# Kernel tuning notes

Measured on AMD Instinct MI355X. Metric: run time of the kernel, lower is better.

## Reference

```python
import jax, jax.numpy as jnp
import numpy as np
from jax import lax

B, T, D, LD, K = 128, 1024, 256, 512, 128
RD = LD + K  # 640 residual-LSTM width
PAD = 15     # (31 - 1) // 2 'same' padding for the LSA location conv


def _gru(x, h, wih, whh, bih, bhh):
    # torch.nn.GRUCell semantics, gate order [r, z, n]
    gi = x @ wih.T + bih
    gh = h @ whh.T + bhh
    ir, iz, inn = jnp.split(gi, 3, axis=-1)
    hr, hz, hn = jnp.split(gh, 3, axis=-1)
    r = jax.nn.sigmoid(ir + hr)
    z = jax.nn.sigmoid(iz + hz)
    n = jnp.tanh(inn + r * hn)
    return (1.0 - z) * n + z * h


def _lstm(x, h, c, wih, whh, bih, bhh):
    # torch.nn.LSTMCell semantics, gate order [i, f, g, o]
    g = x @ wih.T + bih + h @ whh.T + bhh
    i, f, gg, o = jnp.split(g, 4, axis=-1)
    c2 = jax.nn.sigmoid(f) * c + jax.nn.sigmoid(i) * jnp.tanh(gg)
    h2 = jax.nn.sigmoid(o) * jnp.tanh(c2)
    return h2, c2


def _forward(encoder_seq, encoder_seq_proj, prenet_in, attn_hidden, rnn1_h, rnn1_c,
             rnn2_h, rnn2_c, res_h, res_c, context_vec, cumulative, attn_prev,
             fc1_w, fc1_b, fc2_w, fc2_b, gru_wih, gru_whh, gru_bih, gru_bhh,
             conv_w, L_w, L_b, W_w, W_b, v_w, ri_w, ri_b,
             r1_wih, r1_whh, r1_bih, r1_bhh, r2_wih, r2_whh, r2_bih, r2_bhh,
             res_wih, res_whh, res_bih, res_bhh, stop_w, stop_b):
    # PreNet (dropout p = 0 in Decoder.__init__, so pure tanh-MLP)
    p = jnp.tanh(prenet_in @ fc1_w.T + fc1_b)
    prenet_out = jnp.tanh(p @ fc2_w.T + fc2_b)                     # [B, D//2]
    # Attention GRU
    attn_in = jnp.concatenate([context_vec, prenet_out], axis=-1)  # [B, D + D//2]
    attn_h = _gru(attn_in, attn_hidden, gru_wih, gru_whh, gru_bih, gru_bhh)  # [B, D]
    # LSA location-sensitive attention (cumulative/attn_prev are zeros at t=0)
    pq = (attn_h @ W_w.T + W_b)[:, None, :]                        # [B, 1, D]
    loc = jnp.stack([cumulative, attn_prev], axis=1)               # [B, 2, T]
    conv_out = lax.conv_general_dilated(loc, conv_w, (1,), [(PAD, PAD)],
                                        dimension_numbers=('NCH', 'OIH', 'NCH'))  # [B, 32, T]
    ploc = jnp.swapaxes(conv_out, 1, 2) @ L_w.T + L_b              # [B, T, D]
    u = jnp.squeeze(jnp.tanh(pq + encoder_seq_proj + ploc) @ v_w.T, -1)  # [B, T]
    sig = jax.nn.sigmoid(u)
    scores = sig / jnp.sum(sig, axis=1, keepdims=True)             # [B, T]
    cum_new = cumulative + scores
    context = jnp.einsum('bt,btd->bd', scores, encoder_seq)        # [B, D]
    # rnn_input projection + two residual LSTM cells (eval: no zoneout)
    x = jnp.concatenate([context, attn_h], axis=1) @ ri_w.T + ri_b  # [B, LD]
    h1, c1 = _lstm(x, rnn1_h, rnn1_c, r1_wih, r1_whh, r1_bih, r1_bhh)
    x = x + h1
    h2, c2 = _lstm(x, rnn2_h, rnn2_c, r2_wih, r2_whh, r2_bih, r2_bhh)
    x = x + h2
    # 4-layer residual LSTM stack on [prenet_in, x]
    res_x = jnp.concatenate([prenet_in, x], axis=1)                # [B, RD]
    hs, cs = [], []
    for i in range(4):
        hi, ci = _lstm(res_x, res_h[i], res_c[i], res_wih[i], res_whh[i], res_bih[i], res_bhh[i])
        res_x = res_x + hi
        hs.append(hi)
        cs.append(ci)
    cond = res_x                                                   # cond_features [B, RD]
    stop = jax.nn.sigmoid(cond @ stop_w.T + stop_b)                # [B, 1]
    return (cond, stop, scores, attn_h, h1, c1, h2, c2,
            jnp.stack(hs), jnp.stack(cs), context, cum_new)


def setup_inputs() -> dict:
    keys = iter(jax.random.split(jax.random.key(0), 64))
    nxt = lambda: next(keys)
    rn = lambda s: jax.random.normal(nxt(), s, jnp.float32)
    wp = lambda s: rn(s) * 0.02
    return {
        'encoder_seq': rn((B, T, D)),
        'encoder_seq_proj': rn((B, T, D)),
        'prenet_in': rn((B, K)),
        'attn_hidden': rn((B, D)),
        'rnn1_h': rn((B, LD)), 'rnn1_c': rn((B, LD)),
        'rnn2_h': rn((B, LD)), 'rnn2_c': rn((B, LD)),
        'res_h': rn((4, B, RD)), 'res_c': rn((4, B, RD)),
        'context_vec': rn((B, D)),
        'cumulative': jnp.zeros((B, T), jnp.float32),
        'attn_prev': jnp.zeros((B, T), jnp.float32),
        'fc1_w': wp((256, K)), 'fc1_b': jnp.zeros((256,), jnp.float32),
        'fc2_w': wp((D // 2, 256)), 'fc2_b': jnp.zeros((D // 2,), jnp.float32),
        'gru_wih': wp((3 * D, D + D // 2)), 'gru_whh': wp((3 * D, D)),
        'gru_bih': jnp.zeros((3 * D,), jnp.float32), 'gru_bhh': jnp.zeros((3 * D,), jnp.float32),
        'conv_w': wp((32, 2, 31)),
        'L_w': wp((D, 32)), 'L_b': jnp.zeros((D,), jnp.float32),
        'W_w': wp((D, D)), 'W_b': jnp.zeros((D,), jnp.float32),
        'v_w': wp((1, D)),
        'ri_w': wp((LD, 2 * D)), 'ri_b': jnp.zeros((LD,), jnp.float32),
        'r1_wih': wp((4 * LD, LD)), 'r1_whh': wp((4 * LD, LD)),
        'r1_bih': jnp.zeros((4 * LD,), jnp.float32), 'r1_bhh': jnp.zeros((4 * LD,), jnp.float32),
        'r2_wih': wp((4 * LD, LD)), 'r2_whh': wp((4 * LD, LD)),
        'r2_bih': jnp.zeros((4 * LD,), jnp.float32), 'r2_bhh': jnp.zeros((4 * LD,), jnp.float32),
        'res_wih': wp((4, 4 * RD, RD)), 'res_whh': wp((4, 4 * RD, RD)),
        'res_bih': jnp.zeros((4, 4 * RD), jnp.float32), 'res_bhh': jnp.zeros((4, 4 * RD), jnp.float32),
        'stop_w': wp((1, RD)), 'stop_b': jnp.zeros((1,), jnp.float32),
    }


def reference(encoder_seq, encoder_seq_proj, prenet_in, attn_hidden, rnn1_h, rnn1_c,
              rnn2_h, rnn2_c, res_h, res_c, context_vec, cumulative, attn_prev,
              fc1_w, fc1_b, fc2_w, fc2_b, gru_wih, gru_whh, gru_bih, gru_bhh,
              conv_w, L_w, L_b, W_w, W_b, v_w, ri_w, ri_b,
              r1_wih, r1_whh, r1_bih, r1_bhh, r2_wih, r2_whh, r2_bih, r2_bhh,
              res_wih, res_whh, res_bih, res_bhh, stop_w, stop_b):
    return _forward(encoder_seq, encoder_seq_proj, prenet_in, attn_hidden, rnn1_h, rnn1_c,
                    rnn2_h, rnn2_c, res_h, res_c, context_vec, cumulative, attn_prev,
                    fc1_w, fc1_b, fc2_w, fc2_b, gru_wih, gru_whh, gru_bih, gru_bhh,
                    conv_w, L_w, L_b, W_w, W_b, v_w, ri_w, ri_b,
                    r1_wih, r1_whh, r1_bih, r1_bhh, r2_wih, r2_whh, r2_bih, r2_bhh,
                    res_wih, res_whh, res_bih, res_bhh, stop_w, stop_b)
```

## Files before the change

### kernel.cpp

```cpp
#include <hip/hip_runtime.h>

#define DEV __device__ __forceinline__

typedef __attribute__((ext_vector_type(8))) short short8;
typedef __attribute__((ext_vector_type(4))) float f32x4;

DEV float fast_rcp(float x) { return __builtin_amdgcn_rcpf(x); }
DEV float sigm(float x) { return fast_rcp(1.0f + __expf(-x)); }
DEV float tanhf_fast(float x) { return 1.0f - 2.0f * fast_rcp(1.0f + __expf(2.0f * x)); }

DEV short f2bf(float f) {
    unsigned u = __float_as_uint(f);
    unsigned r = (u + 0x7FFFu + ((u >> 16) & 1u)) >> 16;
    return (short)r;
}

__global__ __launch_bounds__(256) void gemm2s_kernel(
    const float* __restrict__ A1, int K1, const float* __restrict__ W1, int ldw1,
    const float* __restrict__ A2, int K2, const float* __restrict__ W2, int ldw2,
    float* __restrict__ Cp, int N, int KS, int KC)
{
    __shared__ float As[2][16][128];
    __shared__ float Ws[2][16][33];
    const int tid = threadIdx.x;
    const int chunk = blockIdx.x % KS;
    const int n0 = (blockIdx.x / KS) * 32;
    const int kbeg = chunk * KC;
    const int nt = KC / 16;
    const int tx = tid & 15, ty = tid >> 4;
    const int lm = tid & 127, lk = (tid >> 7) * 8;

    float acc[16];
#pragma unroll
    for (int i = 0; i < 16; ++i) acc[i] = 0.f;

    float4 ra0, ra1, rw;
    auto load_regs = [&](int k0) {
        const float* A; const float* W; int lda, ldw, kc;
        if (k0 < K1) { A = A1; W = W1; lda = K1; ldw = ldw1; kc = k0; }
        else         { A = A2; W = W2; lda = K2; ldw = ldw2; kc = k0 - K1; }
        ra0 = *(const float4*)(A + (size_t)lm * lda + kc + lk);
        ra1 = *(const float4*)(A + (size_t)lm * lda + kc + lk + 4);
        if (tid < 128) {
            int nl = tid >> 2, kq = (tid & 3) * 4;
            rw = *(const float4*)(W + (size_t)(n0 + nl) * ldw + kc + kq);
        }
    };
    auto store_lds = [&](int buf) {
        As[buf][lk + 0][lm] = ra0.x; As[buf][lk + 1][lm] = ra0.y;
        As[buf][lk + 2][lm] = ra0.z; As[buf][lk + 3][lm] = ra0.w;
        As[buf][lk + 4][lm] = ra1.x; As[buf][lk + 5][lm] = ra1.y;
        As[buf][lk + 6][lm] = ra1.z; As[buf][lk + 7][lm] = ra1.w;
        if (tid < 128) {
            int nl = tid >> 2, kq = (tid & 3) * 4;
            Ws[buf][kq + 0][nl] = rw.x; Ws[buf][kq + 1][nl] = rw.y;
            Ws[buf][kq + 2][nl] = rw.z; Ws[buf][kq + 3][nl] = rw.w;
        }
    };

    load_regs(kbeg);
    store_lds(0);
    __syncthreads();

    for (int it = 0; it < nt; ++it) {
        const int cur = it & 1;
        if (it + 1 < nt) load_regs(kbeg + (it + 1) * 16);
#pragma unroll
        for (int kk = 0; kk < 16; ++kk) {
            float w0 = Ws[cur][kk][tx * 2 + 0];
            float w1 = Ws[cur][kk][tx * 2 + 1];
            float4 x0 = *(const float4*)&As[cur][kk][ty * 8];
            float4 x1 = *(const float4*)&As[cur][kk][ty * 8 + 4];
            acc[0] += x0.x * w0; acc[1] += x0.y * w0;
            acc[2] += x0.z * w0; acc[3] += x0.w * w0;
            acc[4] += x1.x * w0; acc[5] += x1.y * w0;
            acc[6] += x1.z * w0; acc[7] += x1.w * w0;
            acc[8]  += x0.x * w1; acc[9]  += x0.y * w1;
            acc[10] += x0.z * w1; acc[11] += x0.w * w1;
            acc[12] += x1.x * w1; acc[13] += x1.y * w1;
            acc[14] += x1.z * w1; acc[15] += x1.w * w1;
        }
        if (it + 1 < nt) store_lds(cur ^ 1);
        __syncthreads();
    }

    float* Co = Cp + (size_t)chunk * 128 * N;
#pragma unroll
    for (int j = 0; j < 2; ++j) {
        int n = n0 + tx * 2 + j;
#pragma unroll
        for (int i = 0; i < 8; ++i)
            Co[(size_t)(ty * 8 + i) * N + n] = acc[j * 8 + i];
    }
}

__global__ void reduce_act_kernel(const float* __restrict__ p, int KS, int MN,
                                  const float* __restrict__ b,
                                  float* __restrict__ out, int N, int act)
{
    int idx = blockIdx.x * 256 + threadIdx.x;
    if (idx >= MN) return;
    int n = idx % N;
    float v = b ? b[n] : 0.f;
    for (int s = 0; s < KS; ++s) v += p[(size_t)s * MN + idx];
    if (act) v = tanhf_fast(v);
    out[idx] = v;
}

__global__ void gru_gate_kernel(const float* __restrict__ gi_p, int KSi,
                                const float* __restrict__ gh_p, int KSh,
                                const float* __restrict__ bih, const float* __restrict__ bhh,
                                const float* __restrict__ h, float* __restrict__ out)
{
    const size_t MN = 128 * 768;
    int m = blockIdx.x, d = threadIdx.x;
    size_t base = (size_t)m * 768 + d;
    float ir = bih[d], iz = bih[256 + d], in = bih[512 + d];
    for (int s = 0; s < KSi; ++s) {
        const float* p = gi_p + s * MN + base;
        ir += p[0]; iz += p[256]; in += p[512];
    }
    float hr = bhh[d], hz = bhh[256 + d], hn = bhh[512 + d];
    for (int s = 0; s < KSh; ++s) {
        const float* p = gh_p + s * MN + base;
        hr += p[0]; hz += p[256]; hn += p[512];
    }
    float r = sigm(ir + hr);
    float z = sigm(iz + hz);
    float n = tanhf_fast(in + r * hn);
    out[m * 256 + d] = (1.f - z) * n + z * h[m * 256 + d];
}

__global__ void lstm_gate_kernel(const float* __restrict__ gp, int KS,
                                 const float* __restrict__ bih, const float* __restrict__ bhh,
                                 const float* __restrict__ c_in,
                                 float* __restrict__ h_out, float* __restrict__ c_out,
                                 float* __restrict__ xacc, int H)
{
    int d = blockIdx.x * 256 + threadIdx.x;
    int m = blockIdx.y;
    if (d >= H) return;
    const size_t MN = (size_t)128 * 4 * H;
    size_t base = (size_t)m * 4 * H + d;
    float iv = bih[d] + bhh[d];
    float fv = bih[H + d] + bhh[H + d];
    float gv = bih[2 * H + d] + bhh[2 * H + d];
    float ov = bih[3 * H + d] + bhh[3 * H + d];
    for (int s = 0; s < KS; ++s) {
        const float* p = gp + s * MN + base;
        iv += p[0]; fv += p[H]; gv += p[2 * H]; ov += p[3 * H];
    }
    float c2 = sigm(fv) * c_in[m * H + d] + sigm(iv) * tanhf_fast(gv);
    float h2 = sigm(ov) * tanhf_fast(c2);
    h_out[m * H + d] = h2;
    c_out[m * H + d] = c2;
    if (xacc) xacc[m * H + d] += h2;
}

__global__ void lw_bf16_kernel(const float* __restrict__ Lw, short* __restrict__ LwBf)
{
    int i = blockIdx.x * 256 + threadIdx.x;
    LwBf[i] = f2bf(Lw[i]);
}

__global__ __launch_bounds__(256) void attn_u_kernel(
    const float* __restrict__ esp, const float* __restrict__ pq,
    const short* __restrict__ LwBf, const float* __restrict__ Lb,
    const float* __restrict__ vw, const float* __restrict__ cw,
    const float* __restrict__ cum, const float* __restrict__ prev,
    float* __restrict__ sig_out)
{
    const int b = blockIdx.x >> 4;
    const int t0 = (blockIdx.x & 15) << 6;
    const int tid = threadIdx.x;

    __shared__ float cum_s[94], prev_s[94];
    __shared__ float cw_s[2][32][33];
    __shared__ short conv_bf[64 * 32];
    __shared__ short lw_bf[256 * 32];
    __shared__ float pq_s[256], vw_s[256];

    if (tid < 94) {
        int ti = t0 - 15 + tid;
        cum_s[tid] = (ti >= 0 && ti < 1024) ? cum[b * 1024 + ti] : 0.f;
    } else if (tid >= 128 && tid < 222) {
        int i = tid - 128;
        int ti = t0 - 15 + i;
        prev_s[i] = (ti >= 0 && ti < 1024) ? prev[b * 1024 + ti] : 0.f;
    }
    for (int i = tid; i < 2048; i += 256) {
        int which = i >> 10, c = (i >> 5) & 31, k = i & 31;
        cw_s[which][c][k] = (k < 31) ? cw[(c * 2 + which) * 31 + k] : 0.f;
    }
    {
        const int4* src = (const int4*)LwBf;
        int4* dst = (int4*)lw_bf;
#pragma unroll
        for (int k = 0; k < 4; ++k) dst[tid + k * 256] = src[tid + k * 256];
    }
    pq_s[tid] = pq[b * 256 + tid] + Lb[tid];
    vw_s[tid] = vw[tid];
    __syncthreads();

    {
        int c = tid & 31, t8 = (tid >> 5) << 3;
        float a[8] = {0.f, 0.f, 0.f, 0.f, 0.f, 0.f, 0.f, 0.f};
        for (int k = 0; k < 31; ++k) {
            float w0 = cw_s[0][c][k], w1 = cw_s[1][c][k];
#pragma unroll
            for (int j = 0; j < 8; ++j)
                a[j] += w0 * cum_s[t8 + j + k] + w1 * prev_s[t8 + j + k];
        }
#pragma unroll
        for (int j = 0; j < 8; ++j) conv_bf[(t8 + j) * 32 + c] = f2bf(a[j]);
    }
    __syncthreads();

    const int lane = tid & 63, w = tid >> 6;
    const int q = lane >> 4, c16 = lane & 15;
    const int myt = t0 + w * 16 + c16;

    short8 bfrag = *(const short8*)&conv_bf[(w * 16 + c16) * 32 + q * 8];
    const float* er = esp + ((size_t)(b * 1024 + myt) << 8);

    float s = 0.f;
#pragma unroll
    for (int dt = 0; dt < 16; ++dt) {
        short8 afrag = *(const short8*)&lw_bf[(dt * 16 + c16) * 32 + q * 8];
        f32x4 acc = {0.f, 0.f, 0.f, 0.f};
        acc = __builtin_amdgcn_mfma_f32_16x16x32_bf16(afrag, bfrag, acc, 0, 0, 0);
        const int d0 = dt * 16 + q * 4;
        float4 e   = *(const float4*)(er + d0);
        float4 pqv = *(const float4*)&pq_s[d0];
        float4 vwv = *(const float4*)&vw_s[d0];
        s += tanhf_fast(pqv.x + e.x + acc[0]) * vwv.x;
        s += tanhf_fast(pqv.y + e.y + acc[1]) * vwv.y;
        s += tanhf_fast(pqv.z + e.z + acc[2]) * vwv.z;
        s += tanhf_fast(pqv.w + e.w + acc[3]) * vwv.w;
    }
    s += __shfl_xor(s, 16);
    s += __shfl_xor(s, 32);
    if (lane < 16)
        sig_out[b * 1024 + t0 + w * 16 + lane] = sigm(s);
}

__global__ void attn_norm_kernel(const float* __restrict__ sig, const float* __restrict__ cum,
                                 float* __restrict__ scores, float* __restrict__ cum_new,
                                 float* __restrict__ ctx)
{
    __shared__ float red[4];
    int b = blockIdx.x, tid = threadIdx.x;
    float4 sv = *(const float4*)&sig[b * 1024 + tid * 4];
    float s = sv.x + sv.y + sv.z + sv.w;
#pragma unroll
    for (int off = 1; off < 64; off <<= 1) s += __shfl_xor(s, off);
    if ((tid & 63) == 0) red[tid >> 6] = s;
    __syncthreads();
    float inv = fast_rcp(red[0] + red[1] + red[2] + red[3]);
    float4 cv = *(const float4*)&cum[b * 1024 + tid * 4];
    float4 sc = {sv.x * inv, sv.y * inv, sv.z * inv, sv.w * inv};
    *(float4*)&scores[b * 1024 + tid * 4] = sc;
    float4 cn = {cv.x + sc.x, cv.y + sc.y, cv.z + sc.z, cv.w + sc.w};
    *(float4*)&cum_new[b * 1024 + tid * 4] = cn;
    ctx[b * 256 + tid] = 0.f;
}

__global__ void attn_ctx_kernel(const float* __restrict__ scores, const float* __restrict__ es,
                                float* __restrict__ ctx)
{
    __shared__ float sc_s[128];
    int b = blockIdx.x >> 3;
    int tbase = (blockIdx.x & 7) * 128;
    int tid = threadIdx.x;
    if (tid < 128) sc_s[tid] = scores[b * 1024 + tbase + tid];
    __syncthreads();
    float a = 0.f;
    const float* ep = es + ((size_t)(b * 1024 + tbase)) * 256 + tid;
#pragma unroll 4
    for (int tt = 0; tt < 128; ++tt)
        a += sc_s[tt] * ep[(size_t)tt * 256];
    atomicAdd(&ctx[b * 256 + tid], a);
}

__global__ void build_rescat_kernel(const float* __restrict__ pre, const float* __restrict__ x,
                                    float* __restrict__ res)
{
    int idx = blockIdx.x * 256 + threadIdx.x;
    int m = idx / 640, d = idx - m * 640;
    res[idx] = (d < 128) ? pre[m * 128 + d] : x[m * 512 + d - 128];
}

__global__ void copy_kernel(const float* __restrict__ src, float* __restrict__ dst, int n)
{
    int idx = blockIdx.x * 256 + threadIdx.x;
    if (idx < n) dst[idx] = src[idx];
}

__global__ void stop_kernel(const float* __restrict__ res, const float* __restrict__ sw,
                            const float* __restrict__ sb, float* __restrict__ stop)
{
    int m = blockIdx.x, lane = threadIdx.x;
    float s = 0.f;
    for (int k = lane; k < 640; k += 64) s += res[m * 640 + k] * sw[k];
#pragma unroll
    for (int off = 1; off < 64; off <<= 1) s += __shfl_xor(s, off);
    if (lane == 0) stop[m] = sigm(s + sb[0]);
}

extern "C" void kernel_launch(void* const* d_in, const int* in_sizes, int n_in,
                              void* d_out, int out_size, void* d_ws, size_t ws_size,
                              hipStream_t stream)
{
    const float* encoder_seq      = (const float*)d_in[0];
    const float* encoder_seq_proj = (const float*)d_in[1];
    const float* prenet_in        = (const float*)d_in[2];
    const float* attn_hidden      = (const float*)d_in[3];
    const float* rnn1_h  = (const float*)d_in[4];
    const float* rnn1_c  = (const float*)d_in[5];
    const float* rnn2_h  = (const float*)d_in[6];
    const float* rnn2_c  = (const float*)d_in[7];
    const float* res_h   = (const float*)d_in[8];
    const float* res_c   = (const float*)d_in[9];
    const float* context_vec = (const float*)d_in[10];
    const float* cumulative  = (const float*)d_in[11];
    const float* attn_prev   = (const float*)d_in[12];
    const float* fc1_w = (const float*)d_in[13];
    const float* fc1_b = (const float*)d_in[14];
    const float* fc2_w = (const float*)d_in[15];
    const float* fc2_b = (const float*)d_in[16];
    const float* gru_wih = (const float*)d_in[17];
    const float* gru_whh = (const float*)d_in[18];
    const float* gru_bih = (const float*)d_in[19];
    const float* gru_bhh = (const float*)d_in[20];
    const float* conv_w = (const float*)d_in[21];
    const float* L_w = (const float*)d_in[22];
    const float* L_b = (const float*)d_in[23];
    const float* W_w = (const float*)d_in[24];
    const float* W_b = (const float*)d_in[25];
    const float* v_w = (const float*)d_in[26];
    const float* ri_w = (const float*)d_in[27];
    const float* ri_b = (const float*)d_in[28];
    const float* r1_wih = (const float*)d_in[29];
    const float* r1_whh = (const float*)d_in[30];
    const float* r1_bih = (const float*)d_in[31];
    const float* r1_bhh = (const float*)d_in[32];
    const float* r2_wih = (const float*)d_in[33];
    const float* r2_whh = (const float*)d_in[34];
    const float* r2_bih = (const float*)d_in[35];
    const float* r2_bhh = (const float*)d_in[36];
    const float* res_wih = (const float*)d_in[37];
    const float* res_whh = (const float*)d_in[38];
    const float* res_bih = (const float*)d_in[39];
    const float* res_bhh = (const float*)d_in[40];
    const float* stop_w = (const float*)d_in[41];
    const float* stop_b = (const float*)d_in[42];

    float* ws  = (float*)d_ws;
    float* out = (float*)d_out;

    const size_t OFF_P    = 0;
    const size_t OFF_POUT = 32768;
    const size_t OFF_PQ   = 49152;
    const size_t OFF_SIG  = 81920;
    const size_t OFF_X    = 212992;
    const size_t OFF_RES  = 278528;
    const size_t OFF_LWT  = 360448;
    const size_t OFF_PART = 368640;
    const size_t OFF_PARTB = OFF_PART + (size_t)8 * 128 * 768;

    const size_t O_COND   = 0;
    const size_t O_STOP   = 81920;
    const size_t O_SCORES = 82048;
    const size_t O_ATTNH  = 213120;
    const size_t O_H1     = 245888;
    const size_t O_C1     = 311424;
    const size_t O_H2     = 376960;
    const size_t O_C2     = 442496;
    const size_t O_HS     = 508032;
    const size_t O_CS     = 835712;
    const size_t O_CTX    = 1163392;
    const size_t O_CUM    = 1196160;

    short* lwbf = (short*)(ws + OFF_LWT);
    lw_bf16_kernel<<<32, 256, 0, stream>>>(L_w, lwbf);

    gemm2s_kernel<<<8 * 4, 256, 0, stream>>>(prenet_in, 128, fc1_w, 128,
                                             nullptr, 0, nullptr, 0,
                                             ws + OFF_PART, 256, 4, 32);
    reduce_act_kernel<<<128, 256, 0, stream>>>(ws + OFF_PART, 4, 128 * 256, fc1_b,
                                               ws + OFF_P, 256, 1);
    gemm2s_kernel<<<4 * 8, 256, 0, stream>>>(ws + OFF_P, 256, fc2_w, 256,
                                             nullptr, 0, nullptr, 0,
                                             ws + OFF_PART, 128, 8, 32);
    reduce_act_kernel<<<64, 256, 0, stream>>>(ws + OFF_PART, 8, 128 * 128, fc2_b,
                                              ws + OFF_POUT, 128, 1);

    gemm2s_kernel<<<24 * 8, 256, 0, stream>>>(context_vec, 256, gru_wih, 384,
                                              ws + OFF_POUT, 128, gru_wih + 256, 384,
                                              ws + OFF_PART, 768, 8, 48);
    gemm2s_kernel<<<24 * 8, 256, 0, stream>>>(attn_hidden, 256, gru_whh, 256,
                                              nullptr, 0, nullptr, 0,
                                              ws + OFF_PARTB, 768, 8, 32);
    gru_gate_kernel<<<128, 256, 0, stream>>>(ws + OFF_PART, 8, ws + OFF_PARTB, 8,
                                             gru_bih, gru_bhh, attn_hidden, out + O_ATTNH);

    gemm2s_kernel<<<8 * 8, 256, 0, stream>>>(out + O_ATTNH, 256, W_w, 256,
                                             nullptr, 0, nullptr, 0,
                                             ws + OFF_PART, 256, 8, 32);
    reduce_act_kernel<<<128, 256, 0, stream>>>(ws + OFF_PART, 8, 128 * 256, W_b,
                                               ws + OFF_PQ, 256, 0);

    attn_u_kernel<<<2048, 256, 0, stream>>>(encoder_seq_proj, ws + OFF_PQ, lwbf,
                                            L_b, v_w, conv_w, cumulative, attn_prev,
                                            ws + OFF_SIG);
    attn_norm_kernel<<<128, 256, 0, stream>>>(ws + OFF_SIG, cumulative,
                                              out + O_SCORES, out + O_CUM, out + O_CTX);
    attn_ctx_kernel<<<1024, 256, 0, stream>>>(out + O_SCORES, encoder_seq, out + O_CTX);

    gemm2s_kernel<<<16 * 8, 256, 0, stream>>>(out + O_CTX, 256, ri_w, 512,
                                              out + O_ATTNH, 256, ri_w + 256, 512,
                                              ws + OFF_PART, 512, 8, 64);
    reduce_act_kernel<<<256, 256, 0, stream>>>(ws + OFF_PART, 8, 128 * 512, ri_b,
                                               ws + OFF_X, 512, 0);

    gemm2s_kernel<<<64 * 8, 256, 0, stream>>>(ws + OFF_X, 512, r1_wih, 512,
                                              rnn1_h, 512, r1_whh, 512,
                                              ws + OFF_PART, 2048, 8, 128);
    lstm_gate_kernel<<<dim3(2, 128), 256, 0, stream>>>(ws + OFF_PART, 8, r1_bih, r1_bhh,
                                                       rnn1_c, out + O_H1, out + O_C1,
                                                       ws + OFF_X, 512);
    gemm2s_kernel<<<64 * 8, 256, 0, stream>>>(ws + OFF_X, 512, r2_wih, 512,
                                              rnn2_h, 512, r2_whh, 512,
                                              ws + OFF_PART, 2048, 8, 128);
    lstm_gate_kernel<<<dim3(2, 128), 256, 0, stream>>>(ws + OFF_PART, 8, r2_bih, r2_bhh,
                                                       rnn2_c, out + O_H2, out + O_C2,
                                                       ws + OFF_X, 512);

    build_rescat_kernel<<<320, 256, 0, stream>>>(prenet_in, ws + OFF_X, ws + OFF_RES);

    for (int i = 0; i < 4; ++i) {
        const float* wih = res_wih + (size_t)i * 2560 * 640;
        const float* whh = res_whh + (size_t)i * 2560 * 640;
        gemm2s_kernel<<<80 * 8, 256, 0, stream>>>(ws + OFF_RES, 640, wih, 640,
                                                  res_h + (size_t)i * 81920, 640, whh, 640,
                                                  ws + OFF_PART, 2560, 8, 160);
        lstm_gate_kernel<<<dim3(3, 128), 256, 0, stream>>>(ws + OFF_PART, 8,
                                                           res_bih + (size_t)i * 2560,
                                                           res_bhh + (size_t)i * 2560,
                                                           res_c + (size_t)i * 81920,
                                                           out + O_HS + (size_t)i * 81920,
                                                           out + O_CS + (size_t)i * 81920,
                                                           ws + OFF_RES, 640);
    }

    copy_kernel<<<320, 256, 0, stream>>>(ws + OFF_RES, out + O_COND, 128 * 640);
    stop_kernel<<<128, 64, 0, stream>>>(ws + OFF_RES, stop_w, stop_b, out + O_STOP);
}
```

Measured before the change: 660.3 us.

## Switch GEMMs to bf16 MFMA and fuse split-K reductions via last-block counters

Replaces the FP32 SIMT split-K GEMM with a bf16 MFMA 16x16x32 GEMM that converts operands to bf16 while staging them in shared memory. Each GEMM now fuses its split-K reduction and epilogue (bias/tanh, LSTM gates, GRU gates) into the last-arriving block per column group, using atomic counters. This removes the separate reduce, gate, norm, rescat and copy kernels, cutting launch count and partial-buffer round trips. The attention norm is folded into attn_u the same way, and the stop and cond kernels are merged. The cost is bf16 precision loss on all recurrent weights, plus serialized epilogue work in a few blocks.

```diff
diff --git a/kernel.cpp b/kernel.cpp
--- a/kernel.cpp
+++ b/kernel.cpp
@@ -11,156 +11,160 @@
 
 DEV short f2bf(float f) {
     unsigned u = __float_as_uint(f);
-    unsigned r = (u + 0x7FFFu + ((u >> 16) & 1u)) >> 16;
-    return (short)r;
-}
-
-__global__ __launch_bounds__(256) void gemm2s_kernel(
+    return (short)((u + 0x7FFFu + ((u >> 16) & 1u)) >> 16);
+}
+
+__global__ void prep_kernel(const float* __restrict__ Lw, short* __restrict__ lwbf,
+                            const float* __restrict__ pre, float* __restrict__ res,
+                            int* __restrict__ ctr)
+{
+    int i = blockIdx.x * 256 + threadIdx.x;
+    if (i < 512) ctr[i] = 0;
+    if (i < 8192) lwbf[i] = f2bf(Lw[i]);
+    int m = i >> 7, d = i & 127;
+    res[m * 640 + d] = pre[i];
+}
+
+__global__ __launch_bounds__(256) void mfma_gemm(
     const float* __restrict__ A1, int K1, const float* __restrict__ W1, int ldw1,
     const float* __restrict__ A2, int K2, const float* __restrict__ W2, int ldw2,
-    float* __restrict__ Cp, int N, int KS, int KC)
-{
-    __shared__ float As[2][16][128];
-    __shared__ float Ws[2][16][33];
+    float* __restrict__ Cp, int N, int KS, int KC,
+    int mode, int H, int act,
+    const float* __restrict__ b1, const float* __restrict__ b2,
+    const float* __restrict__ c_in, float* __restrict__ h_out, float* __restrict__ c_out,
+    float* __restrict__ xacc, float* __restrict__ xmir,
+    const float* __restrict__ gi_p, int KS_gi, const float* __restrict__ h_prev,
+    int* __restrict__ ctr)
+{
+    __shared__ short As[2][128][32];
+    __shared__ short Ws[2][32][32];
+    __shared__ int lastf;
+
     const int tid = threadIdx.x;
     const int chunk = blockIdx.x % KS;
-    const int n0 = (blockIdx.x / KS) * 32;
-    const int kbeg = chunk * KC;
-    const int nt = KC / 16;
-    const int tx = tid & 15, ty = tid >> 4;
-    const int lm = tid & 127, lk = (tid >> 7) * 8;
-
-    float acc[16];
-#pragma unroll
-    for (int i = 0; i < 16; ++i) acc[i] = 0.f;
-
-    float4 ra0, ra1, rw;
-    auto load_regs = [&](int k0) {
+    const int j = blockIdx.x / KS;
+    const int n0 = j * 32;
+    const int kbeg = chunk * KC, nsteps = KC / 32;
+
+    const int am = tid >> 1, ak = (tid & 1) * 16;
+    const int wn = tid >> 3, wk = (tid & 7) * 4;
+
+    float4 ar0, ar1, ar2, ar3, wr;
+    auto load = [&](int k0) {
         const float* A; const float* W; int lda, ldw, kc;
         if (k0 < K1) { A = A1; W = W1; lda = K1; ldw = ldw1; kc = k0; }
         else         { A = A2; W = W2; lda = K2; ldw = ldw2; kc = k0 - K1; }
-        ra0 = *(const float4*)(A + (size_t)lm * lda + kc + lk);
-        ra1 = *(const float4*)(A + (size_t)lm * lda + kc + lk + 4);
-        if (tid < 128) {
-            int nl = tid >> 2, kq = (tid & 3) * 4;
-            rw = *(const float4*)(W + (size_t)(n0 + nl) * ldw + kc + kq);
+        const float* ap = A + (size_t)am * lda + kc + ak;
+        ar0 = ((const float4*)ap)[0]; ar1 = ((const float4*)ap)[1];
+        ar2 = ((const float4*)ap)[2]; ar3 = ((const float4*)ap)[3];
+        wr = *(const float4*)(W + (size_t)(n0 + wn) * ldw + kc + wk);
+    };
+    auto stos = [&](int buf) {
+        short* arow = &As[buf][am][ak];
+        arow[0] = f2bf(ar0.x); arow[1] = f2bf(ar0.y); arow[2]  = f2bf(ar0.z); arow[3]  = f2bf(ar0.w);
+        arow[4] = f2bf(ar1.x); arow[5] = f2bf(ar1.y); arow[6]  = f2bf(ar1.z); arow[7]  = f2bf(ar1.w);
+        arow[8] = f2bf(ar2.x); arow[9] = f2bf(ar2.y); arow[10] = f2bf(ar2.z); arow[11] = f2bf(ar2.w);
+        arow[12] = f2bf(ar3.x); arow[13] = f2bf(ar3.y); arow[14] = f2bf(ar3.z); arow[15] = f2bf(ar3.w);
+        short* wrow = &Ws[buf][wn][wk];
+        wrow[0] = f2bf(wr.x); wrow[1] = f2bf(wr.y); wrow[2] = f2bf(wr.z); wrow[3] = f2bf(wr.w);
+    };
+
+    const int lane = tid & 63, wv = tid >> 6, q = lane >> 4, r16 = lane & 15;
+    f32x4 acc00 = {0.f, 0.f, 0.f, 0.f}, acc01 = acc00, acc10 = acc00, acc11 = acc00;
+
+    load(kbeg); stos(0); __syncthreads();
+    for (int it = 0; it < nsteps; ++it) {
+        const int cur = it & 1;
+        if (it + 1 < nsteps) load(kbeg + (it + 1) * 32);
+        short8 a0 = *(const short8*)&As[cur][32 * wv + r16][q * 8];
+        short8 a1 = *(const short8*)&As[cur][32 * wv + 16 + r16][q * 8];
+        short8 b0 = *(const short8*)&Ws[cur][r16][q * 8];
+        short8 b1f = *(const short8*)&Ws[cur][16 + r16][q * 8];
+        acc00 = __builtin_amdgcn_mfma_f32_16x16x32_bf16(a0, b0, acc00, 0, 0, 0);
+        acc01 = __builtin_amdgcn_mfma_f32_16x16x32_bf16(a0, b1f, acc01, 0, 0, 0);
+        acc10 = __builtin_amdgcn_mfma_f32_16x16x32_bf16(a1, b0, acc10, 0, 0, 0);
+        acc11 = __builtin_amdgcn_mfma_f32_16x16x32_bf16(a1, b1f, acc11, 0, 0, 0);
+        if (it + 1 < nsteps) stos(cur ^ 1);
+        __syncthreads();
+    }
+
+    {
+        float* Co = Cp + (size_t)chunk * 128 * N;
+        const int mb = 32 * wv + 4 * q;
+#pragma unroll
+        for (int r = 0; r < 4; ++r) {
+            Co[(size_t)(mb + r) * N + n0 + r16]           = acc00[r];
+            Co[(size_t)(mb + r) * N + n0 + 16 + r16]      = acc01[r];
+            Co[(size_t)(mb + 16 + r) * N + n0 + r16]      = acc10[r];
+            Co[(size_t)(mb + 16 + r) * N + n0 + 16 + r16] = acc11[r];
         }
-    };
-    auto store_lds = [&](int buf) {
-        As[buf][lk + 0][lm] = ra0.x; As[buf][lk + 1][lm] = ra0.y;
-        As[buf][lk + 2][lm] = ra0.z; As[buf][lk + 3][lm] = ra0.w;
-        As[buf][lk + 4][lm] = ra1.x; As[buf][lk + 5][lm] = ra1.y;
-        As[buf][lk + 6][lm] = ra1.z; As[buf][lk + 7][lm] = ra1.w;
-        if (tid < 128) {
-            int nl = tid >> 2, kq = (tid & 3) * 4;
-            Ws[buf][kq + 0][nl] = rw.x; Ws[buf][kq + 1][nl] = rw.y;
-            Ws[buf][kq + 2][nl] = rw.z; Ws[buf][kq + 3][nl] = rw.w;
+    }
+    if (mode == 0) return;
+
+    __syncthreads();
+    __threadfence();
+    int grp, tot;
+    if (mode == 1)      { grp = j;            tot = KS; }
+    else if (mode == 2) { grp = j % (H / 32); tot = 4 * KS; }
+    else                { grp = j % 8;        tot = 3 * KS; }
+    if (tid == 0) lastf = (atomicAdd(&ctr[grp], 1) == tot - 1);
+    __syncthreads();
+    if (!lastf) return;
+    __threadfence();
+
+    const int col = grp * 32 + (tid & 31);
+    const int mb2 = (tid >> 5) * 16;
+
+    if (mode == 1) {
+#pragma unroll 4
+        for (int i = 0; i < 16; ++i) {
+            int m = mb2 + i;
+            float v = b1[col];
+            for (int s = 0; s < KS; ++s) v += Cp[(size_t)s * 128 * N + (size_t)m * N + col];
+            if (act) v = tanhf_fast(v);
+            h_out[(size_t)m * N + col] = v;
         }
-    };
-
-    load_regs(kbeg);
-    store_lds(0);
-    __syncthreads();
-
-    for (int it = 0; it < nt; ++it) {
-        const int cur = it & 1;
-        if (it + 1 < nt) load_regs(kbeg + (it + 1) * 16);
-#pragma unroll
-        for (int kk = 0; kk < 16; ++kk) {
-            float w0 = Ws[cur][kk][tx * 2 + 0];
-            float w1 = Ws[cur][kk][tx * 2 + 1];
-            float4 x0 = *(const float4*)&As[cur][kk][ty * 8];
-            float4 x1 = *(const float4*)&As[cur][kk][ty * 8 + 4];
-            acc[0] += x0.x * w0; acc[1] += x0.y * w0;
-            acc[2] += x0.z * w0; acc[3] += x0.w * w0;
-            acc[4] += x1.x * w0; acc[5] += x1.y * w0;
-            acc[6] += x1.z * w0; acc[7] += x1.w * w0;
-            acc[8]  += x0.x * w1; acc[9]  += x0.y * w1;
-            acc[10] += x0.z * w1; acc[11] += x0.w * w1;
-            acc[12] += x1.x * w1; acc[13] += x1.y * w1;
-            acc[14] += x1.z * w1; acc[15] += x1.w * w1;
+    } else if (mode == 2) {
+        for (int i = 0; i < 16; ++i) {
+            int m = mb2 + i;
+            size_t base = (size_t)m * N + col;
+            float iv = b1[col] + b2[col];
+            float fv = b1[H + col] + b2[H + col];
+            float gv = b1[2 * H + col] + b2[2 * H + col];
+            float ov = b1[3 * H + col] + b2[3 * H + col];
+            for (int s = 0; s < KS; ++s) {
+                const float* p = Cp + (size_t)s * 128 * N + base;
+                iv += p[0]; fv += p[H]; gv += p[2 * H]; ov += p[3 * H];
+            }
+            float c2 = sigm(fv) * c_in[(size_t)m * H + col] + sigm(iv) * tanhf_fast(gv);
+            float h2 = sigm(ov) * tanhf_fast(c2);
+            h_out[(size_t)m * H + col] = h2;
+            c_out[(size_t)m * H + col] = c2;
+            if (xacc) {
+                float xv = xacc[(size_t)m * H + col] + h2;
+                xacc[(size_t)m * H + col] = xv;
+                if (xmir) xmir[(size_t)m * 640 + 128 + col] = xv;
+            }
         }
-        if (it + 1 < nt) store_lds(cur ^ 1);
-        __syncthreads();
-    }
-
-    float* Co = Cp + (size_t)chunk * 128 * N;
-#pragma unroll
-    for (int j = 0; j < 2; ++j) {
-        int n = n0 + tx * 2 + j;
-#pragma unroll
-        for (int i = 0; i < 8; ++i)
-            Co[(size_t)(ty * 8 + i) * N + n] = acc[j * 8 + i];
-    }
-}
-
-__global__ void reduce_act_kernel(const float* __restrict__ p, int KS, int MN,
-                                  const float* __restrict__ b,
-                                  float* __restrict__ out, int N, int act)
-{
-    int idx = blockIdx.x * 256 + threadIdx.x;
-    if (idx >= MN) return;
-    int n = idx % N;
-    float v = b ? b[n] : 0.f;
-    for (int s = 0; s < KS; ++s) v += p[(size_t)s * MN + idx];
-    if (act) v = tanhf_fast(v);
-    out[idx] = v;
-}
-
-__global__ void gru_gate_kernel(const float* __restrict__ gi_p, int KSi,
-                                const float* __restrict__ gh_p, int KSh,
-                                const float* __restrict__ bih, const float* __restrict__ bhh,
-                                const float* __restrict__ h, float* __restrict__ out)
-{
-    const size_t MN = 128 * 768;
-    int m = blockIdx.x, d = threadIdx.x;
-    size_t base = (size_t)m * 768 + d;
-    float ir = bih[d], iz = bih[256 + d], in = bih[512 + d];
-    for (int s = 0; s < KSi; ++s) {
-        const float* p = gi_p + s * MN + base;
-        ir += p[0]; iz += p[256]; in += p[512];
-    }
-    float hr = bhh[d], hz = bhh[256 + d], hn = bhh[512 + d];
-    for (int s = 0; s < KSh; ++s) {
-        const float* p = gh_p + s * MN + base;
-        hr += p[0]; hz += p[256]; hn += p[512];
-    }
-    float r = sigm(ir + hr);
-    float z = sigm(iz + hz);
-    float n = tanhf_fast(in + r * hn);
-    out[m * 256 + d] = (1.f - z) * n + z * h[m * 256 + d];
-}
-
-__global__ void lstm_gate_kernel(const float* __restrict__ gp, int KS,
-                                 const float* __restrict__ bih, const float* __restrict__ bhh,
-                                 const float* __restrict__ c_in,
-                                 float* __restrict__ h_out, float* __restrict__ c_out,
-                                 float* __restrict__ xacc, int H)
-{
-    int d = blockIdx.x * 256 + threadIdx.x;
-    int m = blockIdx.y;
-    if (d >= H) return;
-    const size_t MN = (size_t)128 * 4 * H;
-    size_t base = (size_t)m * 4 * H + d;
-    float iv = bih[d] + bhh[d];
-    float fv = bih[H + d] + bhh[H + d];
-    float gv = bih[2 * H + d] + bhh[2 * H + d];
-    float ov = bih[3 * H + d] + bhh[3 * H + d];
-    for (int s = 0; s < KS; ++s) {
-        const float* p = gp + s * MN + base;
-        iv += p[0]; fv += p[H]; gv += p[2 * H]; ov += p[3 * H];
-    }
-    float c2 = sigm(fv) * c_in[m * H + d] + sigm(iv) * tanhf_fast(gv);
-    float h2 = sigm(ov) * tanhf_fast(c2);
-    h_out[m * H + d] = h2;
-    c_out[m * H + d] = c2;
-    if (xacc) xacc[m * H + d] += h2;
-}
-
-__global__ void lw_bf16_kernel(const float* __restrict__ Lw, short* __restrict__ LwBf)
-{
-    int i = blockIdx.x * 256 + threadIdx.x;
-    LwBf[i] = f2bf(Lw[i]);
+    } else {
+        for (int i = 0; i < 16; ++i) {
+            int m = mb2 + i;
+            size_t base = (size_t)m * 768 + col;
+            float ir = b1[col], iz = b1[256 + col], in = b1[512 + col];
+            for (int s = 0; s < KS_gi; ++s) {
+                const float* p = gi_p + (size_t)s * 128 * 768 + base;
+                ir += p[0]; iz += p[256]; in += p[512];
+            }
+            float hr = b2[col], hz = b2[256 + col], hn = b2[512 + col];
+            for (int s = 0; s < KS; ++s) {
+                const float* p = Cp + (size_t)s * 128 * 768 + base;
+                hr += p[0]; hz += p[256]; hn += p[512];
+            }
+            float r = sigm(ir + hr), z = sigm(iz + hz);
+            float n = tanhf_fast(in + r * hn);
+            h_out[m * 256 + col] = (1.f - z) * n + z * h_prev[m * 256 + col];
+        }
+    }
 }
 
 __global__ __launch_bounds__(256) void attn_u_kernel(
@@ -168,7 +172,9 @@
     const short* __restrict__ LwBf, const float* __restrict__ Lb,
     const float* __restrict__ vw, const float* __restrict__ cw,
     const float* __restrict__ cum, const float* __restrict__ prev,
-    float* __restrict__ sig_out)
+    float* __restrict__ sig_out,
+    float* __restrict__ scores, float* __restrict__ cum_new, float* __restrict__ ctx,
+    int* __restrict__ ctr)
 {
     const int b = blockIdx.x >> 4;
     const int t0 = (blockIdx.x & 15) << 6;
@@ -179,6 +185,8 @@
     __shared__ short conv_bf[64 * 32];
     __shared__ short lw_bf[256 * 32];
     __shared__ float pq_s[256], vw_s[256];
+    __shared__ int lastf;
+    __shared__ float red[4];
 
     if (tid < 94) {
         int ti = t0 - 15 + tid;
@@ -208,11 +216,11 @@
         for (int k = 0; k < 31; ++k) {
             float w0 = cw_s[0][c][k], w1 = cw_s[1][c][k];
 #pragma unroll
-            for (int j = 0; j < 8; ++j)
-                a[j] += w0 * cum_s[t8 + j + k] + w1 * prev_s[t8 + j + k];
+            for (int jj = 0; jj < 8; ++jj)
+                a[jj] += w0 * cum_s[t8 + jj + k] + w1 * prev_s[t8 + jj + k];
         }
 #pragma unroll
-        for (int j = 0; j < 8; ++j) conv_bf[(t8 + j) * 32 + c] = f2bf(a[j]);
+        for (int jj = 0; jj < 8; ++jj) conv_bf[(t8 + jj) * 32 + c] = f2bf(a[jj]);
     }
     __syncthreads();
 
@@ -242,19 +250,19 @@
     s += __shfl_xor(s, 32);
     if (lane < 16)
         sig_out[b * 1024 + t0 + w * 16 + lane] = sigm(s);
-}
-
-__global__ void attn_norm_kernel(const float* __restrict__ sig, const float* __restrict__ cum,
-                                 float* __restrict__ scores, float* __restrict__ cum_new,
-                                 float* __restrict__ ctx)
-{
-    __shared__ float red[4];
-    int b = blockIdx.x, tid = threadIdx.x;
-    float4 sv = *(const float4*)&sig[b * 1024 + tid * 4];
-    float s = sv.x + sv.y + sv.z + sv.w;
-#pragma unroll
-    for (int off = 1; off < 64; off <<= 1) s += __shfl_xor(s, off);
-    if ((tid & 63) == 0) red[tid >> 6] = s;
+
+    __syncthreads();
+    __threadfence();
+    if (tid == 0) lastf = (atomicAdd(&ctr[b], 1) == 15);
+    __syncthreads();
+    if (!lastf) return;
+    __threadfence();
+
+    float4 sv = *(const float4*)&sig_out[b * 1024 + tid * 4];
+    float s2 = sv.x + sv.y + sv.z + sv.w;
+#pragma unroll
+    for (int off = 1; off < 64; off <<= 1) s2 += __shfl_xor(s2, off);
+    if ((tid & 63) == 0) red[tid >> 6] = s2;
     __syncthreads();
     float inv = fast_rcp(red[0] + red[1] + red[2] + red[3]);
     float4 cv = *(const float4*)&cum[b * 1024 + tid * 4];
@@ -282,26 +290,17 @@
     atomicAdd(&ctx[b * 256 + tid], a);
 }
 
-__global__ void build_rescat_kernel(const float* __restrict__ pre, const float* __restrict__ x,
-                                    float* __restrict__ res)
-{
-    int idx = blockIdx.x * 256 + threadIdx.x;
-    int m = idx / 640, d = idx - m * 640;
-    res[idx] = (d < 128) ? pre[m * 128 + d] : x[m * 512 + d - 128];
-}
-
-__global__ void copy_kernel(const float* __restrict__ src, float* __restrict__ dst, int n)
-{
-    int idx = blockIdx.x * 256 + threadIdx.x;
-    if (idx < n) dst[idx] = src[idx];
-}
-
-__global__ void stop_kernel(const float* __restrict__ res, const float* __restrict__ sw,
-                            const float* __restrict__ sb, float* __restrict__ stop)
+__global__ void stop_cond_kernel(const float* __restrict__ res, const float* __restrict__ sw,
+                                 const float* __restrict__ sb, float* __restrict__ cond,
+                                 float* __restrict__ stop)
 {
     int m = blockIdx.x, lane = threadIdx.x;
     float s = 0.f;
-    for (int k = lane; k < 640; k += 64) s += res[m * 640 + k] * sw[k];
+    for (int k = lane; k < 640; k += 64) {
+        float v = res[m * 640 + k];
+        cond[m * 640 + k] = v;
+        s += v * sw[k];
+    }
 #pragma unroll
     for (int off = 1; off < 64; off <<= 1) s += __shfl_xor(s, off);
     if (lane == 0) stop[m] = sigm(s + sb[0]);
@@ -365,8 +364,9 @@
     const size_t OFF_X    = 212992;
     const size_t OFF_RES  = 278528;
     const size_t OFF_LWT  = 360448;
-    const size_t OFF_PART = 368640;
-    const size_t OFF_PARTB = OFF_PART + (size_t)8 * 128 * 768;
+    const size_t OFF_CTR  = 364544;
+    const size_t OFF_PART = 365056;
+    const size_t OFF_PARTB = OFF_PART + (size_t)8 * 128 * 2560;
 
     const size_t O_COND   = 0;
     const size_t O_STOP   = 81920;
@@ -382,77 +382,71 @@
     const size_t O_CUM    = 1196160;
 
     short* lwbf = (short*)(ws + OFF_LWT);
-    lw_bf16_kernel<<<32, 256, 0, stream>>>(L_w, lwbf);
-
-    gemm2s_kernel<<<8 * 4, 256, 0, stream>>>(prenet_in, 128, fc1_w, 128,
-                                             nullptr, 0, nullptr, 0,
-                                             ws + OFF_PART, 256, 4, 32);
-    reduce_act_kernel<<<128, 256, 0, stream>>>(ws + OFF_PART, 4, 128 * 256, fc1_b,
-                                               ws + OFF_P, 256, 1);
-    gemm2s_kernel<<<4 * 8, 256, 0, stream>>>(ws + OFF_P, 256, fc2_w, 256,
-                                             nullptr, 0, nullptr, 0,
-                                             ws + OFF_PART, 128, 8, 32);
-    reduce_act_kernel<<<64, 256, 0, stream>>>(ws + OFF_PART, 8, 128 * 128, fc2_b,
-                                              ws + OFF_POUT, 128, 1);
-
-    gemm2s_kernel<<<24 * 8, 256, 0, stream>>>(context_vec, 256, gru_wih, 384,
-                                              ws + OFF_POUT, 128, gru_wih + 256, 384,
-                                              ws + OFF_PART, 768, 8, 48);
-    gemm2s_kernel<<<24 * 8, 256, 0, stream>>>(attn_hidden, 256, gru_whh, 256,
-                                              nullptr, 0, nullptr, 0,
-                                              ws + OFF_PARTB, 768, 8, 32);
-    gru_gate_kernel<<<128, 256, 0, stream>>>(ws + OFF_PART, 8, ws + OFF_PARTB, 8,
-                                             gru_bih, gru_bhh, attn_hidden, out + O_ATTNH);
-
-    gemm2s_kernel<<<8 * 8, 256, 0, stream>>>(out + O_ATTNH, 256, W_w, 256,
-                                             nullptr, 0, nullptr, 0,
-                                             ws + OFF_PART, 256, 8, 32);
-    reduce_act_kernel<<<128, 256, 0, stream>>>(ws + OFF_PART, 8, 128 * 256, W_b,
-                                               ws + OFF_PQ, 256, 0);
-
+    int* ctr = (int*)(ws + OFF_CTR);
+    float* PART = ws + OFF_PART;
+    float* PARTB = ws + OFF_PARTB;
+
+    prep_kernel<<<64, 256, 0, stream>>>(L_w, lwbf, prenet_in, ws + OFF_RES, ctr);
+
+    mfma_gemm<<<8 * 4, 256, 0, stream>>>(prenet_in, 128, fc1_w, 128, nullptr, 0, nullptr, 0,
+                                         PART, 256, 4, 32, 1, 0, 1, fc1_b, nullptr,
+                                         nullptr, ws + OFF_P, nullptr, nullptr, nullptr,
+                                         nullptr, 0, nullptr, ctr + 0);
+    mfma_gemm<<<4 * 8, 256, 0, stream>>>(ws + OFF_P, 256, fc2_w, 256, nullptr, 0, nullptr, 0,
+                                         PART, 128, 8, 32, 1, 0, 1, fc2_b, nullptr,
+                                         nullptr, ws + OFF_POUT, nullptr, nullptr, nullptr,
+                                         nullptr, 0, nullptr, ctr + 8);
+    mfma_gemm<<<24 * 12, 256, 0, stream>>>(context_vec, 256, gru_wih, 384,
+                                           ws + OFF_POUT, 128, gru_wih + 256, 384,
+                                           PARTB, 768, 12, 32, 0, 0, 0, nullptr, nullptr,
+                                           nullptr, nullptr, nullptr, nullptr, nullptr,
+                                           nullptr, 0, nullptr, nullptr);
+    mfma_gemm<<<24 * 8, 256, 0, stream>>>(attn_hidden, 256, gru_whh, 256, nullptr, 0, nullptr, 0,
+                                          PART, 768, 8, 32, 3, 0, 0, gru_bih, gru_bhh,
+                                          nullptr, out + O_ATTNH, nullptr, nullptr, nullptr,
+                                          PARTB, 12, attn_hidden, ctr + 16);
+    mfma_gemm<<<8 * 8, 256, 0, stream>>>(out + O_ATTNH, 256, W_w, 256, nullptr, 0, nullptr, 0,
+                                         PART, 256, 8, 32, 1, 0, 0, W_b, nullptr,
+                                         nullptr, ws + OFF_PQ, nullptr, nullptr, nullptr,
+                                         nullptr, 0, nullptr, ctr + 32);
     attn_u_kernel<<<2048, 256, 0, stream>>>(encoder_seq_proj, ws + OFF_PQ, lwbf,
                                             L_b, v_w, conv_w, cumulative, attn_prev,
-                                            ws + OFF_SIG);
-    attn_norm_kernel<<<128, 256, 0, stream>>>(ws + OFF_SIG, cumulative,
-                                              out + O_SCORES, out + O_CUM, out + O_CTX);
+                                            ws + OFF_SIG, out + O_SCORES, out + O_CUM,
+                                            out + O_CTX, ctr + 256);
     attn_ctx_kernel<<<1024, 256, 0, stream>>>(out + O_SCORES, encoder_seq, out + O_CTX);
 
-    gemm2s_kernel<<<16 * 8, 256, 0, stream>>>(out + O_CTX, 256, ri_w, 512,
-                                              out + O_ATTNH, 256, ri_w + 256, 512,
-                                              ws + OFF_PART, 512, 8, 64);
-    reduce_act_kernel<<<256, 256, 0, stream>>>(ws + OFF_PART, 8, 128 * 512, ri_b,
-                                               ws + OFF_X, 512, 0);
-
-    gemm2s_kernel<<<64 * 8, 256, 0, stream>>>(ws + OFF_X, 512, r1_wih, 512,
-                                              rnn1_h, 512, r1_whh, 512,
-                                              ws + OFF_PART, 2048, 8, 128);
-    lstm_gate_kernel<<<dim3(2, 128), 256, 0, stream>>>(ws + OFF_PART, 8, r1_bih, r1_bhh,
-                                                       rnn1_c, out + O_H1, out + O_C1,
-                                                       ws + OFF_X, 512);
-    gemm2s_kernel<<<64 * 8, 256, 0, stream>>>(ws + OFF_X, 512, r2_wih, 512,
-                                              rnn2_h, 512, r2_whh, 512,
-                                              ws + OFF_PART, 2048, 8, 128);
-    lstm_gate_kernel<<<dim3(2, 128), 256, 0, stream>>>(ws + OFF_PART, 8, r2_bih, r2_bhh,
-                                                       rnn2_c, out + O_H2, out + O_C2,
-                                                       ws + OFF_X, 512);
-
-    build_rescat_kernel<<<320, 256, 0, stream>>>(prenet_in, ws + OFF_X, ws + OFF_RES);
-
+    mfma_gemm<<<16 * 8, 256, 0, stream>>>(out + O_CTX, 256, ri_w, 512,
+                                          out + O_ATTNH, 256, ri_w + 256, 512,
+                                          PART, 512, 8, 64, 1, 0, 0, ri_b, nullptr,
+                                          nullptr, ws + OFF_X, nullptr, nullptr, nullptr,
+                                          nullptr, 0, nullptr, ctr + 48);
+    mfma_gemm<<<64 * 8, 256, 0, stream>>>(ws + OFF_X, 512, r1_wih, 512,
+                                          rnn1_h, 512, r1_whh, 512,
+                                          PART, 2048, 8, 128, 2, 512, 0, r1_bih, r1_bhh,
+                                          rnn1_c, out + O_H1, out + O_C1,
+                                          ws + OFF_X, nullptr,
+                                          nullptr, 0, nullptr, ctr + 64);
+    mfma_gemm<<<64 * 8, 256, 0, stream>>>(ws + OFF_X, 512, r2_wih, 512,
+                                          rnn2_h, 512, r2_whh, 512,
+                                          PART, 2048, 8, 128, 2, 512, 0, r2_bih, r2_bhh,
+                                          rnn2_c, out + O_H2, out + O_C2,
+                                          ws + OFF_X, ws + OFF_RES,
+                                          nullptr, 0, nullptr, ctr + 96);
     for (int i = 0; i < 4; ++i) {
-        const float* wih = res_wih + (size_t)i * 2560 * 640;
-        const float* whh = res_whh + (size_t)i * 2560 * 640;
-        gemm2s_kernel<<<80 * 8, 256, 0, stream>>>(ws + OFF_RES, 640, wih, 640,
-                                                  res_h + (size_t)i * 81920, 640, whh, 640,
-                                                  ws + OFF_PART, 2560, 8, 160);
-        lstm_gate_kernel<<<dim3(3, 128), 256, 0, stream>>>(ws + OFF_PART, 8,
-                                                           res_bih + (size_t)i * 2560,
-                                                           res_bhh + (size_t)i * 2560,
-                                                           res_c + (size_t)i * 81920,
-                                                           out + O_HS + (size_t)i * 81920,
-                                                           out + O_CS + (size_t)i * 81920,
-                                                           ws + OFF_RES, 640);
-    }
-
-    copy_kernel<<<320, 256, 0, stream>>>(ws + OFF_RES, out + O_COND, 128 * 640);
-    stop_kernel<<<128, 64, 0, stream>>>(ws + OFF_RES, stop_w, stop_b, out + O_STOP);
-}
+        mfma_gemm<<<80 * 8, 256, 0, stream>>>(ws + OFF_RES, 640,
+                                              res_wih + (size_t)i * 2560 * 640, 640,
+                                              res_h + (size_t)i * 81920, 640,
+                                              res_whh + (size_t)i * 2560 * 640, 640,
+                                              PART, 2560, 8, 160, 2, 640, 0,
+                                              res_bih + (size_t)i * 2560,
+                                              res_bhh + (size_t)i * 2560,
+                                              res_c + (size_t)i * 81920,
+                                              out + O_HS + (size_t)i * 81920,
+                                              out + O_CS + (size_t)i * 81920,
+                                              ws + OFF_RES, nullptr,
+                                              nullptr, 0, nullptr, ctr + 128 + 32 * i);
+    }
+
+    stop_cond_kernel<<<128, 64, 0, stream>>>(ws + OFF_RES, stop_w, stop_b,
+                                             out + O_COND, out + O_STOP);
+}
```

New measurement: 1.891 ms. +186.4%, slower.
